# Optimization experiments

Hardware: AMD Instinct MI355X
Metric: run time of the kernel (lower is better)

## Reference

```python
import jax, jax.numpy as jnp
import numpy as np

D_MODEL = 512
NUM_HEADS = 8
D_K = D_MODEL // NUM_HEADS
SCALE = 1.0 / np.sqrt(D_K).astype(np.float32)


def _relative_shift(x):
    # x: (B, H, S, P) pos scores from Q @ P^T; Transformer-XL shift trick.
    b, h, s, p = x.shape
    x = jnp.pad(x, ((0, 0), (0, 0), (0, 0), (1, 0)))   # (B,H,S,P+1)
    x = x.reshape(b, h, p + 1, s)[:, :, 1:, :]          # drop first row
    x = x.reshape(b, h, s, p)[:, :, :, :s]
    return x


def setup_inputs() -> dict:
    key = jax.random.key(0)
    ks = jax.random.split(key, 10)
    B, S = 4, 2048
    glorot = lambda k: jax.random.uniform(
        k, (D_MODEL, D_MODEL), jnp.float32,
        -np.sqrt(6.0 / (2 * D_MODEL)), np.sqrt(6.0 / (2 * D_MODEL)))
    return {
        "inputs": jax.random.normal(ks[0], (B, S, D_MODEL), jnp.float32),
        "pos_enc": jax.random.normal(ks[1], (1, S, D_MODEL), jnp.float32),
        "W_q": glorot(ks[2]),
        "W_k": glorot(ks[3]),
        "W_v": glorot(ks[4]),
        "W_o": glorot(ks[5]),
        "W_pos": glorot(ks[6]),
        "u_bias": jnp.zeros((NUM_HEADS, D_K), jnp.float32),
        "v_bias": jnp.zeros((NUM_HEADS, D_K), jnp.float32),
    }


def reference(inputs, pos_enc, W_q, W_k, W_v, W_o, W_pos, u_bias, v_bias):
    B, S, _ = inputs.shape
    split = lambda x, b: x.reshape(b, S, NUM_HEADS, D_K).transpose(0, 2, 1, 3)
    Q = split(inputs @ W_q, B)        # (B,H,S,dk)
    K = split(inputs @ W_k, B)
    V = split(inputs @ W_v, B)
    P = split(pos_enc @ W_pos, 1)      # (1,H,S,dk)
    u = u_bias[None, :, None, :]
    v = v_bias[None, :, None, :]
    content_score = jnp.einsum('bhid,bhjd->bhij', Q + u, K)
    pos_score = jnp.einsum('bhid,xhjd->bhij', Q + v, P)  # broadcast over batch
    pos_score = _relative_shift(pos_score)
    scores = (content_score + pos_score) * SCALE
    attn = jax.nn.softmax(scores, axis=-1)  # no dropout (inference)
    context = jnp.einsum('bhij,bhjd->bhid', attn, V)
    context = context.transpose(0, 2, 1, 3).reshape(B, S, D_MODEL)
    return context @ W_o
```

## Files before the change

kernel.cpp:

```cpp
#include <hip/hip_runtime.h>
#include <hip/hip_bf16.h>
#include <math.h>

#define SEQ 2048
#define NH 8
#define DK 64
#define DM 512
#define RSCALE 0.125f
#define PPAD (SEQ + 128)
#define POFF 64
#define KSTR 72
#define PSTR 36

typedef unsigned short ushortT;
typedef short s16x8 __attribute__((ext_vector_type(8)));
typedef float f32x4 __attribute__((ext_vector_type(4)));

#define MFMA16 __builtin_amdgcn_mfma_f32_16x16x32_bf16

static __device__ __forceinline__ ushortT f2bf(float x) {
  __hip_bfloat16 h = __float2bfloat16(x);
  ushortT u;
  __builtin_memcpy(&u, &h, 2);
  return u;
}

static __device__ __forceinline__ f32x4 exp4(f32x4 g) {
  f32x4 r;
  r[0] = __expf(g[0]); r[1] = __expf(g[1]);
  r[2] = __expf(g[2]); r[3] = __expf(g[3]);
  return r;
}

static __device__ __forceinline__ s16x8 pack8(const float* p) {
  ushortT u[8];
#pragma unroll
  for (int i = 0; i < 8; ++i) u[i] = f2bf(p[i]);
  s16x8 out;
  __builtin_memcpy(&out, u, 16);
  return out;
}

__global__ __launch_bounds__(256)
void cast_in(const float* __restrict__ X, const float* __restrict__ PE,
             ushortT* __restrict__ Xb, ushortT* __restrict__ PEb) {
  const size_t i4 = (size_t)blockIdx.x * 256 + threadIdx.x;
  const size_t NX = (size_t)4 * SEQ * DM / 4;
  const float4 v = (i4 < NX) ? *(const float4*)(X + i4 * 4)
                             : *(const float4*)(PE + (i4 - NX) * 4);
  ushortT o[4] = {f2bf(v.x), f2bf(v.y), f2bf(v.z), f2bf(v.w)};
  ushortT* dst = (i4 < NX) ? (Xb + i4 * 4) : (PEb + (i4 - NX) * 4);
  *(ulonglong1*)dst = *(ulonglong1*)o;
}

__global__ __launch_bounds__(256)
void transpose_w(const float* __restrict__ w0, const float* __restrict__ w1,
                 const float* __restrict__ w2, const float* __restrict__ w3,
                 const float* __restrict__ w4, ushortT* __restrict__ out) {
  __shared__ float ts[32][33];
  const int z = blockIdx.z;
  const float* w = (z == 0) ? w0 : (z == 1) ? w1 : (z == 2) ? w2 : (z == 3) ? w3 : w4;
  ushortT* o = out + (size_t)z * DM * DM;
  const int k0 = blockIdx.x * 32, n0 = blockIdx.y * 32;
  const int tx = threadIdx.x, ty = threadIdx.y;
#pragma unroll
  for (int i = 0; i < 4; ++i)
    ts[ty + i * 8][tx] = w[(size_t)(k0 + ty + i * 8) * DM + n0 + tx];
  __syncthreads();
#pragma unroll
  for (int i = 0; i < 4; ++i)
    o[(size_t)(n0 + ty + i * 8) * DM + k0 + tx] = f2bf(ts[tx][ty + i * 8]);
}

__global__ __launch_bounds__(256)
void gemm_mfma(const ushortT* __restrict__ A, const ushortT* __restrict__ Bt,
               const float* __restrict__ ubv, const float* __restrict__ vbv,
               ushortT* __restrict__ qu, ushortT* __restrict__ qv,
               ushortT* __restrict__ kb, ushortT* __restrict__ vt,
               float* __restrict__ of, int mode) {
  const int w = threadIdx.x >> 6, lane = threadIdx.x & 63;
  const int c = lane & 15, q = lane >> 4;
  const int m0 = blockIdx.x * 64;
  const int n0 = blockIdx.y * 128 + w * 32;

  const ushortT* Ab = A + (size_t)m0 * DM + q * 8;
  const ushortT* Bb = Bt + (size_t)n0 * DM + q * 8;

  f32x4 acc[4][2];
#pragma unroll
  for (int mt = 0; mt < 4; ++mt)
#pragma unroll
    for (int nt = 0; nt < 2; ++nt) acc[mt][nt] = (f32x4){0.f, 0.f, 0.f, 0.f};

  s16x8 a[4], bfr[2], an[4], bn[2];
#pragma unroll
  for (int mt = 0; mt < 4; ++mt) a[mt] = *(const s16x8*)(Ab + (size_t)(mt * 16 + c) * DM);
#pragma unroll
  for (int nt = 0; nt < 2; ++nt) bfr[nt] = *(const s16x8*)(Bb + (size_t)(nt * 16 + c) * DM);

  for (int k0 = 0; k0 < DM; k0 += 32) {
    if (k0 + 32 < DM) {
#pragma unroll
      for (int mt = 0; mt < 4; ++mt)
        an[mt] = *(const s16x8*)(Ab + (size_t)(mt * 16 + c) * DM + k0 + 32);
#pragma unroll
      for (int nt = 0; nt < 2; ++nt)
        bn[nt] = *(const s16x8*)(Bb + (size_t)(nt * 16 + c) * DM + k0 + 32);
    }
#pragma unroll
    for (int mt = 0; mt < 4; ++mt)
#pragma unroll
      for (int nt = 0; nt < 2; ++nt)
        acc[mt][nt] = MFMA16(a[mt], bfr[nt], acc[mt][nt], 0, 0, 0);
#pragma unroll
    for (int mt = 0; mt < 4; ++mt) a[mt] = an[mt];
#pragma unroll
    for (int nt = 0; nt < 2; ++nt) bfr[nt] = bn[nt];
  }

#pragma unroll
  for (int mt = 0; mt < 4; ++mt)
#pragma unroll
    for (int nt = 0; nt < 2; ++nt)
#pragma unroll
      for (int r = 0; r < 4; ++r) {
        const int gm = m0 + mt * 16 + q * 4 + r;
        const int gn = n0 + nt * 16 + c;
        const float v = acc[mt][nt][r];
        const int bb = gm >> 11, s = gm & (SEQ - 1);
        if (mode == 0) {
          const int z = gn >> 9, gn5 = gn & 511;
          const int h = gn5 >> 6, d = gn5 & 63;
          if (z == 0) {
            const size_t base = (((size_t)bb * NH + h) * SEQ + s) * DK + d;
            qu[base] = f2bf((v + ubv[gn5]) * RSCALE);
            qv[base] = f2bf((v + vbv[gn5]) * RSCALE);
          } else if (z == 1) {
            kb[(((size_t)bb * NH + h) * SEQ + s) * DK + d] = f2bf(v);
          } else {
            vt[(((size_t)bb * NH + h) * DK + d) * SEQ + s] = f2bf(v);
          }
        } else if (mode == 3) {
          const int h = gn >> 6, d = gn & 63;
          qu[((size_t)h * PPAD + POFF + gm) * DK + d] = f2bf(v);
        } else {
          of[(size_t)gm * DM + gn] = v;
        }
      }
}

static __device__ __forceinline__ f32x4 band_gemm(const ushortT* pb, int tile,
                                                  int c, int q, s16x8 a0, s16x8 a1) {
  const ushortT* pc = pb + (ptrdiff_t)(tile * 16 + c) * DK + q * 8;
  f32x4 G = {0.f, 0.f, 0.f, 0.f};
  G = MFMA16(a0, *(const s16x8*)pc, G, 0, 0, 0);
  G = MFMA16(a1, *(const s16x8*)(pc + 32), G, 0, 0, 0);
  return G;
}

__global__ __launch_bounds__(256, 3)
void attn_mfma(const ushortT* __restrict__ Qu, const ushortT* __restrict__ Qv,
               const ushortT* __restrict__ Kb, const ushortT* __restrict__ Vt,
               const ushortT* __restrict__ Pp, ushortT* __restrict__ ctxb) {
  const int n = blockIdx.x;
  const int xcd = n & 7, idx = n >> 3;
  const int b = idx >> 5, iblk = idx & 31;
  const int h = xcd, bh = b * 8 + h;
  const int tid = threadIdx.x;
  const int w = tid >> 6, lane = tid & 63;
  const int c = lane & 15, q = lane >> 4;
  const int i0 = iblk * 64;
  const int iw = i0 + w * 16;

  __shared__ ushortT Ks[64][KSTR];
  __shared__ ushortT Vs[64][KSTR];
  __shared__ float Ps[4][16][PSTR];
  __shared__ float E1[4][16][PSTR];
  __shared__ float Lb[4][16];

  const ushortT* Qub = Qu + ((size_t)bh * SEQ + iw) * DK;
  const ushortT* Qvb = Qv + ((size_t)bh * SEQ + iw) * DK;
  const ushortT* Kbh = Kb + (size_t)bh * SEQ * DK;
  const ushortT* Vbh = Vt + (size_t)bh * DK * SEQ;
  const ushortT* Ph  = Pp + ((size_t)h * PPAD + POFF) * DK;

  const s16x8 qu0 = *(const s16x8*)(Qub + (size_t)c * DK + q * 8);
  const s16x8 qu1 = *(const s16x8*)(Qub + (size_t)c * DK + 32 + q * 8);
  s16x8 qv0 = *(const s16x8*)(Qvb + (size_t)c * DK + q * 8);
  s16x8 qv1 = *(const s16x8*)(Qvb + (size_t)c * DK + 32 + q * 8);

  int sl[4], b0r[4];
#pragma unroll
  for (int r = 0; r < 4; ++r) {
    const int m = q * 4 + r;
    const int pp0 = c - m + 15;
    sl[r] = q * 16 + (pp0 & 15);
    b0r[r] = pp0 >> 4;
  }

  f32x4 O[4];
#pragma unroll
  for (int r = 0; r < 4; ++r) O[r] = (f32x4){0.f, 0.f, 0.f, 0.f};
  float lrow = 0.f;
  f32x4 e[3];
  bool hv1 = false, hv2 = false;
  const int jt = iw & ~31;
  const int m_w = q * 4;

  {
    const ushortT* gk = Kbh;
    uint4 k0v = *(const uint4*)(gk + tid * 8);
    uint4 k1v = *(const uint4*)(gk + 2048 + tid * 8);
    const ushortT* gv = Vbh + (size_t)(tid >> 2) * SEQ + (tid & 3) * 16;
    uint4 v0v = *(const uint4*)gv;
    uint4 v1v = *(const uint4*)(gv + 8);
    *(uint4*)&Ks[tid >> 3][(tid & 7) * 8] = k0v;
    *(uint4*)&Ks[32 + (tid >> 3)][(tid & 7) * 8] = k1v;
    *(uint4*)&Vs[tid >> 2][(tid & 3) * 16] = v0v;
    *(uint4*)&Vs[tid >> 2][(tid & 3) * 16 + 8] = v1v;
  }
  __syncthreads();

#define WRITE_PS(S0v, S1v)                                                    \
  _Pragma("unroll")                                                           \
  for (int r = 0; r < 4; ++r) {                                               \
    Ps[w][m_w + r][c] = __expf((S0v)[r]);                                     \
    Ps[w][m_w + r][16 + c] = __expf((S1v)[r]);                                \
  }

#define WRITE_BAND(ev)                                                        \
  _Pragma("unroll")                                                           \
  for (int t = 0; t < 3; ++t)                                                 \
    _Pragma("unroll")                                                         \
    for (int r = 0; r < 4; ++r) {                                             \
      const int kcol = t * 16 + c + (m_w + r) - 15;                           \
      if (kcol >= 0 && kcol < 32) E1[w][m_w + r][kcol] = (ev)[t][r];          \
    }

#define PV_FACTOR(jl)                                                         \
  {                                                                           \
    const float* psr = &Ps[w][c][q * 8];                                      \
    const float* e1r = &E1[w][c][q * 8];                                      \
    float4 pA = *(const float4*)(psr), pB = *(const float4*)(psr + 4);        \
    float4 fA = *(const float4*)(e1r), fB = *(const float4*)(e1r + 4);        \
    float pr[8] = {pA.x * fA.x, pA.y * fA.y, pA.z * fA.z, pA.w * fA.w,        \
                   pB.x * fB.x, pB.y * fB.y, pB.z * fB.z, pB.w * fB.w};       \
    lrow += pr[0] + pr[1] + pr[2] + pr[3] + pr[4] + pr[5] + pr[6] + pr[7];    \
    const s16x8 pa = pack8(pr);                                               \
    _Pragma("unroll")                                                         \
    for (int dt = 0; dt < 4; ++dt) {                                          \
      const s16x8 vb = *(const s16x8*)&Vs[dt * 16 + c][(jl) + q * 8];         \
      O[dt] = MFMA16(pa, vb, O[dt], 0, 0, 0);                                 \
    }                                                                         \
  }

#define PV_PLAIN(jl)                                                          \
  {                                                                           \
    const float* psr = &Ps[w][c][q * 8];                                      \
    float4 pA = *(const float4*)(psr), pB = *(const float4*)(psr + 4);        \
    float pr[8] = {pA.x, pA.y, pA.z, pA.w, pB.x, pB.y, pB.z, pB.w};           \
    lrow += pr[0] + pr[1] + pr[2] + pr[3] + pr[4] + pr[5] + pr[6] + pr[7];    \
    const s16x8 pa = pack8(pr);                                               \
    _Pragma("unroll")                                                         \
    for (int dt = 0; dt < 4; ++dt) {                                          \
      const s16x8 vb = *(const s16x8*)&Vs[dt * 16 + c][(jl) + q * 8];         \
      O[dt] = MFMA16(pa, vb, O[dt], 0, 0, 0);                                 \
    }                                                                         \
  }

  for (int ch = 0; ch < 32; ++ch) {
    const bool more = (ch + 1) < 32;
    uint4 k0v, k1v, v0v, v1v;
    if (more) {
      const ushortT* gk = Kbh + (size_t)(ch + 1) * 64 * DK;
      k0v = *(const uint4*)(gk + tid * 8);
      k1v = *(const uint4*)(gk + 2048 + tid * 8);
      const ushortT* gv = Vbh + (size_t)(tid >> 2) * SEQ + (ch + 1) * 64 + (tid & 3) * 16;
      v0v = *(const uint4*)gv;
      v1v = *(const uint4*)(gv + 8);
    }
#pragma unroll
    for (int t = 0; t < 2; ++t) {
      const int j0 = ch * 64 + t * 32;
      const int jl = t * 32;
      const int drel = j0 - iw;
      f32x4 S0 = {0.f, 0.f, 0.f, 0.f}, S1 = {0.f, 0.f, 0.f, 0.f};
      {
        const ushortT* kp = &Ks[jl + c][q * 8];
        S0 = MFMA16(qu0, *(const s16x8*)kp, S0, 0, 0, 0);
        S0 = MFMA16(qu1, *(const s16x8*)(kp + 32), S0, 0, 0, 0);
        const ushortT* kp2 = &Ks[jl + 16 + c][q * 8];
        S1 = MFMA16(qu0, *(const s16x8*)kp2, S1, 0, 0, 0);
        S1 = MFMA16(qu1, *(const s16x8*)(kp2 + 32), S1, 0, 0, 0);
      }
      if (j0 < jt) {
        const ushortT* pb1 = Ph + (ptrdiff_t)(drel + SEQ - 16) * DK;
        if (hv1) e[0] = e[2];
        else { e[0] = exp4(band_gemm(pb1, 0, c, q, qv0, qv1)); hv1 = true; }
        e[1] = exp4(band_gemm(pb1, 1, c, q, qv0, qv1));
        e[2] = exp4(band_gemm(pb1, 2, c, q, qv0, qv1));
        WRITE_BAND(e)
        WRITE_PS(S0, S1)
        PV_FACTOR(jl)
      } else if (j0 < jt + 64) {
        f32x4 g1[3], g2[3];
        const ushortT* pb1 = Ph + (ptrdiff_t)(drel + SEQ - 16) * DK;
        g1[0] = band_gemm(pb1, 0, c, q, qv0, qv1);
        g1[1] = band_gemm(pb1, 1, c, q, qv0, qv1);
        g1[2] = band_gemm(pb1, 2, c, q, qv0, qv1);
        {
          const s16x8 qw0 = *(const s16x8*)(Qvb + (size_t)(c + 1) * DK + q * 8);
          const s16x8 qw1 = *(const s16x8*)(Qvb + (size_t)(c + 1) * DK + 32 + q * 8);
          const ushortT* pb2 = Ph + (ptrdiff_t)(drel - 17) * DK;
          g2[0] = band_gemm(pb2, 0, c, q, qw0, qw1);
          g2[1] = band_gemm(pb2, 1, c, q, qw0, qw1);
          g2[2] = band_gemm(pb2, 2, c, q, qw0, qw1);
        }
#pragma unroll
        for (int r = 0; r < 4; ++r) {
          const int m = q * 4 + r;
          const float a0 = __shfl(g1[0][r], sl[r]);
          const float a1 = __shfl(g1[1][r], sl[r]);
          const float a2 = __shfl(g1[2][r], sl[r]);
          const float xA0 = b0r[r] ? a1 : a0;
          const float xA1 = b0r[r] ? a2 : a1;
          const float b0 = __shfl(g2[0][r], sl[r]);
          const float b1 = __shfl(g2[1][r], sl[r]);
          const float b2 = __shfl(g2[2][r], sl[r]);
          const float xB0 = b0r[r] ? b1 : b0;
          const float xB1 = b0r[r] ? b2 : b1;
          const int dlt0 = drel + c - m;
          const float pos0 = (dlt0 <= 0) ? xA0 : ((dlt0 == 1) ? 0.f : xB0);
          const int dlt1 = dlt0 + 16;
          const float pos1 = (dlt1 <= 0) ? xA1 : ((dlt1 == 1) ? 0.f : xB1);
          Ps[w][m][c] = __expf(S0[r] + pos0);
          Ps[w][m][16 + c] = __expf(S1[r] + pos1);
        }
        PV_PLAIN(jl)
      } else {
        if (!hv2) {
          qv0 = *(const s16x8*)(Qvb + (size_t)(c + 1) * DK + q * 8);
          qv1 = *(const s16x8*)(Qvb + (size_t)(c + 1) * DK + 32 + q * 8);
        }
        const ushortT* pb2 = Ph + (ptrdiff_t)(drel - 17) * DK;
        if (hv2) e[0] = e[2];
        else { e[0] = exp4(band_gemm(pb2, 0, c, q, qv0, qv1)); hv2 = true; }
        e[1] = exp4(band_gemm(pb2, 1, c, q, qv0, qv1));
        e[2] = exp4(band_gemm(pb2, 2, c, q, qv0, qv1));
        WRITE_BAND(e)
        WRITE_PS(S0, S1)
        PV_FACTOR(jl)
      }
    }
    __syncthreads();
    if (more) {
      *(uint4*)&Ks[tid >> 3][(tid & 7) * 8] = k0v;
      *(uint4*)&Ks[32 + (tid >> 3)][(tid & 7) * 8] = k1v;
      *(uint4*)&Vs[tid >> 2][(tid & 3) * 16] = v0v;
      *(uint4*)&Vs[tid >> 2][(tid & 3) * 16 + 8] = v1v;
    }
    __syncthreads();
  }

  lrow += __shfl_xor(lrow, 16);
  lrow += __shfl_xor(lrow, 32);
  if (q == 0) Lb[w][c] = lrow;
  float inv[4];
#pragma unroll
  for (int r = 0; r < 4; ++r) inv[r] = 1.0f / Lb[w][q * 4 + r];
#pragma unroll
  for (int dt = 0; dt < 4; ++dt)
#pragma unroll
    for (int r = 0; r < 4; ++r) {
      const int i = iw + q * 4 + r;
      ctxb[((size_t)b * SEQ + i) * DM + h * DK + dt * 16 + c] = f2bf(O[dt][r] * inv[r]);
    }
}

extern "C" void kernel_launch(void* const* d_in, const int* in_sizes, int n_in,
                              void* d_out, int out_size, void* d_ws, size_t ws_size,
                              hipStream_t stream) {
  (void)in_sizes; (void)n_in; (void)out_size; (void)ws_size;
  const float* X   = (const float*)d_in[0];
  const float* PE  = (const float*)d_in[1];
  const float* Wq  = (const float*)d_in[2];
  const float* Wk  = (const float*)d_in[3];
  const float* Wv  = (const float*)d_in[4];
  const float* Wo  = (const float*)d_in[5];
  const float* Wp  = (const float*)d_in[6];
  const float* ubv = (const float*)d_in[7];
  const float* vbv = (const float*)d_in[8];

  const size_t NX = (size_t)4 * SEQ * DM;
  const size_t NP = (size_t)SEQ * DM;
  const size_t NW = (size_t)DM * DM;
  ushortT* Xb  = (ushortT*)d_ws;
  ushortT* PEb = Xb + NX;
  ushortT* Wt  = PEb + NP;
  ushortT* qu  = Wt + 5 * NW;
  ushortT* qv  = qu + NX;
  ushortT* kb  = qv + NX;
  ushortT* vt  = kb + NX;
  ushortT* pp  = vt + NX;
  ushortT* ctx = pp + (size_t)NH * PPAD * DK;
  float* outp = (float*)d_out;

  hipLaunchKernelGGL(cast_in, dim3((NX + NP) / 4 / 256), dim3(256), 0, stream, X, PE, Xb, PEb);
  hipLaunchKernelGGL(transpose_w, dim3(16, 16, 5), dim3(32, 8), 0, stream, Wq, Wk, Wv, Wp, Wo, Wt);
  dim3 blk(256);
  hipLaunchKernelGGL(gemm_mfma, dim3(128, 12), blk, 0, stream, Xb, Wt, ubv, vbv,
                     qu, qv, kb, vt, (float*)nullptr, 0);
  hipLaunchKernelGGL(gemm_mfma, dim3(32, 4), blk, 0, stream, PEb, Wt + 3 * NW, ubv, vbv,
                     pp, (ushortT*)nullptr, (ushortT*)nullptr, (ushortT*)nullptr, (float*)nullptr, 3);
  hipLaunchKernelGGL(attn_mfma, dim3(1024), blk, 0, stream, qu, qv, kb, vt, pp, ctx);
  hipLaunchKernelGGL(gemm_mfma, dim3(128, 4), blk, 0, stream, ctx, Wt + 4 * NW, ubv, vbv,
                     (ushortT*)nullptr, (ushortT*)nullptr, (ushortT*)nullptr, (ushortT*)nullptr, outp, 4);
}
```

Before: 414.5 us.

## Compute content scores transposed and permute V to skip the Ps LDS round-trip

The QK^T MFMA now has its operands swapped, so each lane holds score values in the layout the PV MFMA's A-operand expects. The V^T columns are written in an interleaved order (pinv) so these register-resident scores line up with V in shared memory. This removes the write of exp(scores) to the Ps shared buffer and the read back. The diagonal-band path now uses two exponentiated band tables (E1/E2) multiplied in, replacing the shuffle-based gather. The cost is extra LDS for E2, more exponentials in the band tiles, and a permuted-index dependency between the projection kernel and the attention kernel.

```diff
diff --git a/kernel.cpp b/kernel.cpp
--- a/kernel.cpp
+++ b/kernel.cpp
@@ -39,6 +39,10 @@
   s16x8 out;
   __builtin_memcpy(&out, u, 16);
   return out;
+}
+
+static __device__ __forceinline__ int pinv(int j) {
+  return (j < 16) ? ((j >> 2) * 8 + (j & 3)) : (((j >> 2) - 4) * 8 + 4 + (j & 3));
 }
 
 __global__ __launch_bounds__(256)
@@ -138,7 +142,8 @@
           } else if (z == 1) {
             kb[(((size_t)bb * NH + h) * SEQ + s) * DK + d] = f2bf(v);
           } else {
-            vt[(((size_t)bb * NH + h) * DK + d) * SEQ + s] = f2bf(v);
+            const int s_il = (s & ~31) | pinv(s & 31);
+            vt[(((size_t)bb * NH + h) * DK + d) * SEQ + s_il] = f2bf(v);
           }
         } else if (mode == 3) {
           const int h = gn >> 6, d = gn & 63;
@@ -174,8 +179,8 @@
 
   __shared__ ushortT Ks[64][KSTR];
   __shared__ ushortT Vs[64][KSTR];
-  __shared__ float Ps[4][16][PSTR];
   __shared__ float E1[4][16][PSTR];
+  __shared__ float E2[4][16][PSTR];
   __shared__ float Lb[4][16];
 
   const ushortT* Qub = Qu + ((size_t)bh * SEQ + iw) * DK;
@@ -189,14 +194,10 @@
   s16x8 qv0 = *(const s16x8*)(Qvb + (size_t)c * DK + q * 8);
   s16x8 qv1 = *(const s16x8*)(Qvb + (size_t)c * DK + 32 + q * 8);
 
-  int sl[4], b0r[4];
-#pragma unroll
-  for (int r = 0; r < 4; ++r) {
-    const int m = q * 4 + r;
-    const int pp0 = c - m + 15;
-    sl[r] = q * 16 + (pp0 & 15);
-    b0r[r] = pp0 >> 4;
-  }
+  int joff[8];
+#pragma unroll
+  for (int jj = 0; jj < 8; ++jj)
+    joff[jj] = (jj < 4) ? (4 * q + jj) : (16 + 4 * q + (jj - 4));
 
   f32x4 O[4];
 #pragma unroll
@@ -221,44 +222,17 @@
   }
   __syncthreads();
 
-#define WRITE_PS(S0v, S1v)                                                    \
-  _Pragma("unroll")                                                           \
-  for (int r = 0; r < 4; ++r) {                                               \
-    Ps[w][m_w + r][c] = __expf((S0v)[r]);                                     \
-    Ps[w][m_w + r][16 + c] = __expf((S1v)[r]);                                \
-  }
-
-#define WRITE_BAND(ev)                                                        \
+#define WRITE_BAND(ARR, ev)                                                   \
   _Pragma("unroll")                                                           \
   for (int t = 0; t < 3; ++t)                                                 \
     _Pragma("unroll")                                                         \
     for (int r = 0; r < 4; ++r) {                                             \
       const int kcol = t * 16 + c + (m_w + r) - 15;                           \
-      if (kcol >= 0 && kcol < 32) E1[w][m_w + r][kcol] = (ev)[t][r];          \
-    }
-
-#define PV_FACTOR(jl)                                                         \
+      if (kcol >= 0 && kcol < 32) ARR[w][m_w + r][pinv(kcol)] = (ev)[t][r];   \
+    }
+
+#define PV_FROM(pr, jl)                                                       \
   {                                                                           \
-    const float* psr = &Ps[w][c][q * 8];                                      \
-    const float* e1r = &E1[w][c][q * 8];                                      \
-    float4 pA = *(const float4*)(psr), pB = *(const float4*)(psr + 4);        \
-    float4 fA = *(const float4*)(e1r), fB = *(const float4*)(e1r + 4);        \
-    float pr[8] = {pA.x * fA.x, pA.y * fA.y, pA.z * fA.z, pA.w * fA.w,        \
-                   pB.x * fB.x, pB.y * fB.y, pB.z * fB.z, pB.w * fB.w};       \
-    lrow += pr[0] + pr[1] + pr[2] + pr[3] + pr[4] + pr[5] + pr[6] + pr[7];    \
-    const s16x8 pa = pack8(pr);                                               \
-    _Pragma("unroll")                                                         \
-    for (int dt = 0; dt < 4; ++dt) {                                          \
-      const s16x8 vb = *(const s16x8*)&Vs[dt * 16 + c][(jl) + q * 8];         \
-      O[dt] = MFMA16(pa, vb, O[dt], 0, 0, 0);                                 \
-    }                                                                         \
-  }
-
-#define PV_PLAIN(jl)                                                          \
-  {                                                                           \
-    const float* psr = &Ps[w][c][q * 8];                                      \
-    float4 pA = *(const float4*)(psr), pB = *(const float4*)(psr + 4);        \
-    float pr[8] = {pA.x, pA.y, pA.z, pA.w, pB.x, pB.y, pB.z, pB.w};           \
     lrow += pr[0] + pr[1] + pr[2] + pr[3] + pr[4] + pr[5] + pr[6] + pr[7];    \
     const s16x8 pa = pack8(pr);                                               \
     _Pragma("unroll")                                                         \
@@ -286,12 +260,12 @@
       const int drel = j0 - iw;
       f32x4 S0 = {0.f, 0.f, 0.f, 0.f}, S1 = {0.f, 0.f, 0.f, 0.f};
       {
-        const ushortT* kp = &Ks[jl + c][q * 8];
-        S0 = MFMA16(qu0, *(const s16x8*)kp, S0, 0, 0, 0);
-        S0 = MFMA16(qu1, *(const s16x8*)(kp + 32), S0, 0, 0, 0);
-        const ushortT* kp2 = &Ks[jl + 16 + c][q * 8];
-        S1 = MFMA16(qu0, *(const s16x8*)kp2, S1, 0, 0, 0);
-        S1 = MFMA16(qu1, *(const s16x8*)(kp2 + 32), S1, 0, 0, 0);
+        const ushortT* ka = &Ks[jl + c][q * 8];
+        S0 = MFMA16(*(const s16x8*)ka, qu0, S0, 0, 0, 0);
+        S0 = MFMA16(*(const s16x8*)(ka + 32), qu1, S0, 0, 0, 0);
+        const ushortT* ka2 = &Ks[jl + 16 + c][q * 8];
+        S1 = MFMA16(*(const s16x8*)ka2, qu0, S1, 0, 0, 0);
+        S1 = MFMA16(*(const s16x8*)(ka2 + 32), qu1, S1, 0, 0, 0);
       }
       if (j0 < jt) {
         const ushortT* pb1 = Ph + (ptrdiff_t)(drel + SEQ - 16) * DK;
@@ -299,44 +273,49 @@
         else { e[0] = exp4(band_gemm(pb1, 0, c, q, qv0, qv1)); hv1 = true; }
         e[1] = exp4(band_gemm(pb1, 1, c, q, qv0, qv1));
         e[2] = exp4(band_gemm(pb1, 2, c, q, qv0, qv1));
-        WRITE_BAND(e)
-        WRITE_PS(S0, S1)
-        PV_FACTOR(jl)
+        WRITE_BAND(E1, e)
+        const float* e1r = &E1[w][c][q * 8];
+        float4 fA = *(const float4*)e1r, fB = *(const float4*)(e1r + 4);
+        float pr[8] = {__expf(S0[0]) * fA.x, __expf(S0[1]) * fA.y,
+                       __expf(S0[2]) * fA.z, __expf(S0[3]) * fA.w,
+                       __expf(S1[0]) * fB.x, __expf(S1[1]) * fB.y,
+                       __expf(S1[2]) * fB.z, __expf(S1[3]) * fB.w};
+        PV_FROM(pr, jl)
       } else if (j0 < jt + 64) {
-        f32x4 g1[3], g2[3];
-        const ushortT* pb1 = Ph + (ptrdiff_t)(drel + SEQ - 16) * DK;
-        g1[0] = band_gemm(pb1, 0, c, q, qv0, qv1);
-        g1[1] = band_gemm(pb1, 1, c, q, qv0, qv1);
-        g1[2] = band_gemm(pb1, 2, c, q, qv0, qv1);
+        {
+          const ushortT* pb1 = Ph + (ptrdiff_t)(drel + SEQ - 16) * DK;
+          f32x4 t1[3];
+          t1[0] = exp4(band_gemm(pb1, 0, c, q, qv0, qv1));
+          t1[1] = exp4(band_gemm(pb1, 1, c, q, qv0, qv1));
+          t1[2] = exp4(band_gemm(pb1, 2, c, q, qv0, qv1));
+          WRITE_BAND(E1, t1)
+        }
         {
           const s16x8 qw0 = *(const s16x8*)(Qvb + (size_t)(c + 1) * DK + q * 8);
           const s16x8 qw1 = *(const s16x8*)(Qvb + (size_t)(c + 1) * DK + 32 + q * 8);
           const ushortT* pb2 = Ph + (ptrdiff_t)(drel - 17) * DK;
-          g2[0] = band_gemm(pb2, 0, c, q, qw0, qw1);
-          g2[1] = band_gemm(pb2, 1, c, q, qw0, qw1);
-          g2[2] = band_gemm(pb2, 2, c, q, qw0, qw1);
+          f32x4 t2[3];
+          t2[0] = exp4(band_gemm(pb2, 0, c, q, qw0, qw1));
+          t2[1] = exp4(band_gemm(pb2, 1, c, q, qw0, qw1));
+          t2[2] = exp4(band_gemm(pb2, 2, c, q, qw0, qw1));
+          WRITE_BAND(E2, t2)
         }
-#pragma unroll
-        for (int r = 0; r < 4; ++r) {
-          const int m = q * 4 + r;
-          const float a0 = __shfl(g1[0][r], sl[r]);
-          const float a1 = __shfl(g1[1][r], sl[r]);
-          const float a2 = __shfl(g1[2][r], sl[r]);
-          const float xA0 = b0r[r] ? a1 : a0;
-          const float xA1 = b0r[r] ? a2 : a1;
-          const float b0 = __shfl(g2[0][r], sl[r]);
-          const float b1 = __shfl(g2[1][r], sl[r]);
-          const float b2 = __shfl(g2[2][r], sl[r]);
-          const float xB0 = b0r[r] ? b1 : b0;
-          const float xB1 = b0r[r] ? b2 : b1;
-          const int dlt0 = drel + c - m;
-          const float pos0 = (dlt0 <= 0) ? xA0 : ((dlt0 == 1) ? 0.f : xB0);
-          const int dlt1 = dlt0 + 16;
-          const float pos1 = (dlt1 <= 0) ? xA1 : ((dlt1 == 1) ? 0.f : xB1);
-          Ps[w][m][c] = __expf(S0[r] + pos0);
-          Ps[w][m][16 + c] = __expf(S1[r] + pos1);
+        const float* e1r = &E1[w][c][q * 8];
+        const float* e2r = &E2[w][c][q * 8];
+        float4 aA = *(const float4*)e1r, aB = *(const float4*)(e1r + 4);
+        float4 bA = *(const float4*)e2r, bB = *(const float4*)(e2r + 4);
+        float f1[8] = {aA.x, aA.y, aA.z, aA.w, aB.x, aB.y, aB.z, aB.w};
+        float f2[8] = {bA.x, bA.y, bA.z, bA.w, bB.x, bB.y, bB.z, bB.w};
+        float es[8] = {__expf(S0[0]), __expf(S0[1]), __expf(S0[2]), __expf(S0[3]),
+                       __expf(S1[0]), __expf(S1[1]), __expf(S1[2]), __expf(S1[3])};
+        float pr[8];
+#pragma unroll
+        for (int jj = 0; jj < 8; ++jj) {
+          const int dlt = drel + joff[jj] - c;
+          const float f = (dlt <= 0) ? f1[jj] : ((dlt == 1) ? 1.0f : f2[jj]);
+          pr[jj] = es[jj] * f;
         }
-        PV_PLAIN(jl)
+        PV_FROM(pr, jl)
       } else {
         if (!hv2) {
           qv0 = *(const s16x8*)(Qvb + (size_t)(c + 1) * DK + q * 8);
@@ -347,9 +326,14 @@
         else { e[0] = exp4(band_gemm(pb2, 0, c, q, qv0, qv1)); hv2 = true; }
         e[1] = exp4(band_gemm(pb2, 1, c, q, qv0, qv1));
         e[2] = exp4(band_gemm(pb2, 2, c, q, qv0, qv1));
-        WRITE_BAND(e)
-        WRITE_PS(S0, S1)
-        PV_FACTOR(jl)
+        WRITE_BAND(E1, e)
+        const float* e1r = &E1[w][c][q * 8];
+        float4 fA = *(const float4*)e1r, fB = *(const float4*)(e1r + 4);
+        float pr[8] = {__expf(S0[0]) * fA.x, __expf(S0[1]) * fA.y,
+                       __expf(S0[2]) * fA.z, __expf(S0[3]) * fA.w,
+                       __expf(S1[0]) * fB.x, __expf(S1[1]) * fB.y,
+                       __expf(S1[2]) * fB.z, __expf(S1[3]) * fB.w};
+        PV_FROM(pr, jl)
       }
     }
     __syncthreads();
```

New measurement: 408.1 us. No clear change (-1.5%).
